# Kernel optimization log

Hardware: AMD Instinct MI355X
Metric: run time of the kernel (lower is better)

Reference implementation:

```python
import jax, jax.numpy as jnp
import numpy as np

EPS = 1e-6
KH, KW = 3, 3
SH, SW = 1, 1


def _unfold(x, kh, kw, sh, sw):
    # x: [N, C, H, W] -> patches [N, C, kh*kw, L], L = ox*oy (torch.nn.Unfold layout)
    N, C, H, W = x.shape
    ox = (H - kh) // sh + 1
    oy = (W - kw) // sw + 1
    pats = [x[:, :, i:i + sh * ox:sh, j:j + sw * oy:sw]
            for i in range(kh) for j in range(kw)]
    p = jnp.stack(pats, axis=2)  # [N, C, K, ox, oy]
    return p.reshape(N, C, kh * kw, ox * oy), ox, oy


def setup_inputs() -> dict:
    key = jax.random.key(0)
    kx, k1, k2 = jax.random.split(key, 3)
    x = jax.random.uniform(kx, (32, 2, 64, 64, 64), dtype=jnp.float32)
    w1 = jax.random.uniform(k1, (64, KH * KW), dtype=jnp.float32)
    w2 = jax.random.uniform(k2, (128, 64), dtype=jnp.float32)
    return {"x": x, "w1": w1, "w2": w2}


def reference(x, w1, w2):
    B = x.shape[0]
    out_ch = w2.shape[0]
    xr = x[:, 0]  # rotation plane [B, C, H, W]
    xa = x[:, 1]  # magnitude plane

    pr, ox, oy = _unfold(xr, KH, KW, SH, SW)  # [B, C, K, L]
    pa, _, _ = _unfold(xa, KH, KW, SH, SW)

    # weightNormalize1: squared weights normalized by GLOBAL sum (rot branch)
    w1_glob = w1 ** 2 / jnp.sum(w1 ** 2)
    w2_glob = w2 ** 2 / jnp.sum(w2 ** 2)
    # weightNormalize (drop_prob=0): squared weights normalized PER ROW (abs branch)
    w1_row = w1 ** 2 / jnp.sum(w1 ** 2, axis=1, keepdims=True)
    w2_row = w2 ** 2 / jnp.sum(w2 ** 2, axis=1, keepdims=True)

    # rotation branch: two weighted contractions
    rot = jnp.einsum('bckl,ck->bcl', pr, w1_glob)          # [B, C, L]
    out_rot = jnp.einsum('bcl,oc->bol', rot, w2_glob)      # [B, O, L]
    out_rot = out_rot.reshape(B, 1, out_ch, ox, oy)

    # magnitude branch: log -> weighted contractions -> exp
    la = jnp.log(pa + EPS)                                  # [B, C, K, L]
    a1 = jnp.einsum('bckl,ck->bcl', la, w1_row)             # [B, C, L]
    out_abs = jnp.exp(jnp.einsum('bcl,oc->bol', a1, w2_row))
    out_abs = out_abs.reshape(B, 1, out_ch, ox, oy)

    return jnp.concatenate([out_rot, out_abs], axis=1)  # [B, 2, O, ox, oy]
```

## Files before the change

kernel.cpp:

```cpp
#include <hip/hip_runtime.h>
#include <cstdint>
#include <cstddef>

#define EPSF 1e-6f

typedef __attribute__((ext_vector_type(4))) float f32x4;
typedef __attribute__((ext_vector_type(8))) short s16x8;
typedef union { s16x8 v; unsigned u[4]; } s16x8u;

static __device__ __forceinline__ unsigned short f2bf(float f) {
    unsigned u = __float_as_uint(f);
    u += 0x7FFFu + ((u >> 16) & 1u);
    return (unsigned short)(u >> 16);
}
static __device__ __forceinline__ float bf2f(unsigned short h) {
    return __uint_as_float(((unsigned)h) << 16);
}
static __device__ __forceinline__ unsigned packHL(float v) {
    unsigned short h = f2bf(v);
    float r = v - bf2f(h);
    unsigned short l = f2bf(r);
    return ((unsigned)h << 16) | (unsigned)l;
}

__global__ __launch_bounds__(256) void prep_weights(const float* __restrict__ w1,
                                                    const float* __restrict__ w2,
                                                    float* __restrict__ ws) {
    __shared__ float part1[4], part2[4];
    __shared__ float s1row[64];
    __shared__ float s2row[128];
    __shared__ float tot[2];

    const int t = threadIdx.x;
    const int ln = t & 63;
    const int wv = t >> 6;

    float s1 = 0.f;
    for (int i = t; i < 64 * 9; i += 256) { float v = w1[i]; s1 += v * v; }
    float s2 = 0.f;
    const float4* w2v = (const float4*)w2;
    for (int i = t; i < 2048; i += 256) {
        float4 v = w2v[i];
        s2 += v.x * v.x + v.y * v.y + v.z * v.z + v.w * v.w;
    }
    #pragma unroll
    for (int d = 32; d > 0; d >>= 1) {
        s1 += __shfl_down(s1, d);
        s2 += __shfl_down(s2, d);
    }
    if (ln == 0) { part1[wv] = s1; part2[wv] = s2; }

    if (t < 64) {
        float rs = 0.f;
        #pragma unroll
        for (int k = 0; k < 9; ++k) { float v = w1[t * 9 + k]; rs += v * v; }
        s1row[t] = rs;
    } else if (t < 192) {
        const int o = t - 64;
        float rs = 0.f;
        const float4* p = (const float4*)(w2 + o * 64);
        #pragma unroll
        for (int k = 0; k < 16; ++k) {
            float4 v = p[k];
            rs += v.x * v.x + v.y * v.y + v.z * v.z + v.w * v.w;
        }
        s2row[o] = rs;
    }
    __syncthreads();
    if (t == 0) tot[0] = part1[0] + part1[1] + part1[2] + part1[3];
    if (t == 1) tot[1] = part2[0] + part2[1] + part2[2] + part2[3];
    __syncthreads();

    const float t1 = tot[0];
    const float t2 = tot[1];
    for (int i = t; i < 64 * 9; i += 256) {
        const int c = i / 9;
        const int k = i - c * 9;
        const int idx = (c >> 4) * 144 + (c & 3) * 36 + ((c >> 2) & 3) * 9 + k;
        float q = w1[i] * w1[i];
        ws[idx] = q / t1;
        ws[576 + idx] = q / s1row[c];
    }
    unsigned* wsu = (unsigned*)ws;
    for (int i = t; i < 8192; i += 256) {
        float q = w2[i] * w2[i];
        wsu[1152 + i]        = packHL(q / t2);
        wsu[1152 + 8192 + i] = packHL(q / s2row[i >> 6]);
    }
}

__global__ __launch_bounds__(256) void conv_fused(const float* __restrict__ x,
                                                  const float* __restrict__ ws,
                                                  float* __restrict__ out) {
    const int h = blockIdx.x;
    const int branch = blockIdx.y;
    const int b = blockIdx.z;
    const int t = threadIdx.x;
    const int lane = t & 63;
    const int wv = __builtin_amdgcn_readfirstlane(t >> 6);
    const int lm = lane & 15;
    const int quad = lane >> 4;
    const int c4 = lm;
    const int chsub = quad;

    __shared__ unsigned rotT[64 * 65];

    const float* __restrict__ w1t = ws + branch * 576;
    const unsigned* __restrict__ w2p = (const unsigned*)ws + 1152 + branch * 8192;
    const float* __restrict__ xb = x + (size_t)(b * 2 + branch) * (64 * 4096);

    const float* xrow = xb + h * 64 + 4 * c4;
    #pragma unroll 2
    for (int cg = 0; cg < 4; ++cg) {
        const int c = wv * 16 + cg * 4 + chsub;
        const float* xp = xrow + c * 4096;
        float4 v0 = *(const float4*)xp;
        float4 v1 = *(const float4*)(xp + 64);
        float4 v2 = *(const float4*)(xp + 128);
        if (branch) {
            v0.x = __logf(v0.x + EPSF); v0.y = __logf(v0.y + EPSF);
            v0.z = __logf(v0.z + EPSF); v0.w = __logf(v0.w + EPSF);
            v1.x = __logf(v1.x + EPSF); v1.y = __logf(v1.y + EPSF);
            v1.z = __logf(v1.z + EPSF); v1.w = __logf(v1.w + EPSF);
            v2.x = __logf(v2.x + EPSF); v2.y = __logf(v2.y + EPSF);
            v2.z = __logf(v2.z + EPSF); v2.w = __logf(v2.w + EPSF);
        }
        const float sx0 = __shfl_down(v0.x, 1), sy0 = __shfl_down(v0.y, 1);
        const float sx1 = __shfl_down(v1.x, 1), sy1 = __shfl_down(v1.y, 1);
        const float sx2 = __shfl_down(v2.x, 1), sy2 = __shfl_down(v2.y, 1);
        const float* wc = w1t + wv * 144 + chsub * 36 + cg * 9;
        const float w0 = wc[0], w1_ = wc[1], w2_ = wc[2];
        const float w3 = wc[3], w4 = wc[4], w5 = wc[5];
        const float w6 = wc[6], w7 = wc[7], w8 = wc[8];
        float p0 = v0.x * w0 + v0.y * w1_ + v0.z * w2_
                 + v1.x * w3 + v1.y * w4  + v1.z * w5
                 + v2.x * w6 + v2.y * w7  + v2.z * w8;
        float p1 = v0.y * w0 + v0.z * w1_ + v0.w * w2_
                 + v1.y * w3 + v1.z * w4  + v1.w * w5
                 + v2.y * w6 + v2.z * w7  + v2.w * w8;
        float p2 = v0.z * w0 + v0.w * w1_ + sx0 * w2_
                 + v1.z * w3 + v1.w * w4  + sx1 * w5
                 + v2.z * w6 + v2.w * w7  + sx2 * w8;
        float p3 = v0.w * w0 + sx0 * w1_ + sy0 * w2_
                 + v1.w * w3 + sx1 * w4  + sy1 * w5
                 + v2.w * w6 + sx2 * w7  + sy2 * w8;
        unsigned* rp = &rotT[(4 * c4) * 65 + c];
        rp[0]   = packHL(p0);
        rp[65]  = packHL(p1);
        rp[130] = packHL(p2);
        rp[195] = packHL(p3);
    }

    unsigned araw[2][2][8];
    #pragma unroll
    for (int mt = 0; mt < 2; ++mt) {
        #pragma unroll
        for (int kk = 0; kk < 2; ++kk) {
            const unsigned* p = w2p + (wv * 32 + mt * 16 + lm) * 64 + kk * 32 + quad * 8;
            #pragma unroll
            for (int j = 0; j < 8; ++j) araw[mt][kk][j] = p[j];
        }
    }
    __syncthreads();

    s16x8u aH[2][2], aL[2][2];
    #pragma unroll
    for (int mt = 0; mt < 2; ++mt)
        #pragma unroll
        for (int kk = 0; kk < 2; ++kk)
            #pragma unroll
            for (int j2 = 0; j2 < 4; ++j2) {
                unsigned u0 = araw[mt][kk][2 * j2], u1 = araw[mt][kk][2 * j2 + 1];
                aH[mt][kk].u[j2] = __builtin_amdgcn_perm(u1, u0, 0x07060302u);
                aL[mt][kk].u[j2] = __builtin_amdgcn_perm(u1, u0, 0x05040100u);
            }

    f32x4 acc[2][4];
    #pragma unroll
    for (int mt = 0; mt < 2; ++mt)
        #pragma unroll
        for (int nt = 0; nt < 4; ++nt)
            acc[mt][nt] = (f32x4){0.f, 0.f, 0.f, 0.f};

    #pragma unroll
    for (int nt = 0; nt < 4; ++nt) {
        #pragma unroll
        for (int kk = 0; kk < 2; ++kk) {
            const unsigned* lp = &rotT[(nt * 16 + lm) * 65 + kk * 32 + quad * 8];
            s16x8u bH, bL;
            #pragma unroll
            for (int j2 = 0; j2 < 4; ++j2) {
                unsigned u0 = lp[2 * j2], u1 = lp[2 * j2 + 1];
                bH.u[j2] = __builtin_amdgcn_perm(u1, u0, 0x07060302u);
                bL.u[j2] = __builtin_amdgcn_perm(u1, u0, 0x05040100u);
            }
            #pragma unroll
            for (int mt = 0; mt < 2; ++mt) {
                acc[mt][nt] = __builtin_amdgcn_mfma_f32_16x16x32_bf16(aH[mt][kk].v, bH.v, acc[mt][nt], 0, 0, 0);
                acc[mt][nt] = __builtin_amdgcn_mfma_f32_16x16x32_bf16(aH[mt][kk].v, bL.v, acc[mt][nt], 0, 0, 0);
                acc[mt][nt] = __builtin_amdgcn_mfma_f32_16x16x32_bf16(aL[mt][kk].v, bH.v, acc[mt][nt], 0, 0, 0);
            }
        }
    }

    #pragma unroll
    for (int mt = 0; mt < 2; ++mt) {
        const int oc0 = wv * 32 + mt * 16 + quad * 4;
        #pragma unroll
        for (int nt = 0; nt < 4; ++nt) {
            const int px = nt * 16 + lm;
            if (px < 62) {
                const size_t base =
                    ((size_t)((b * 2 + branch) * 128 + oc0)) * 3844 + (size_t)h * 62 + px;
                #pragma unroll
                for (int r = 0; r < 4; ++r) {
                    float v = acc[mt][nt][r];
                    if (branch) v = __expf(v);
                    out[base + (size_t)r * 3844] = v;
                }
            }
        }
    }
}

extern "C" void kernel_launch(void* const* d_in, const int* in_sizes, int n_in,
                              void* d_out, int out_size, void* d_ws, size_t ws_size,
                              hipStream_t stream) {
    const float* x  = (const float*)d_in[0];
    const float* w1 = (const float*)d_in[1];
    const float* w2 = (const float*)d_in[2];
    float* out = (float*)d_out;
    float* ws  = (float*)d_ws;

    prep_weights<<<1, 256, 0, stream>>>(w1, w2, ws);

    dim3 grid(62, 2, 32);
    conv_fused<<<grid, 256, 0, stream>>>(x, ws, out);
}
```

Measured before the change: 219.1 us.

## Process two output rows per block, split weight prep into parallel kernels

The conv kernel now computes two output rows per block. It loads four input rows and reuses the middle two across both rows, and doubles the LDS tile and the MFMA N-tiles. The grid is reordered with batch on x and paired rows on z, and output stores become nontemporal. The single-block weight prep is split into two multi-block kernels: one computes row sums, and one packs the weights and recomputes the global sums from the stored row sums. This adds a kernel launch and raises LDS and register use per block, with the launch bound set to 4 waves per EU.

```diff
diff --git a/kernel.cpp b/kernel.cpp
--- a/kernel.cpp
+++ b/kernel.cpp
@@ -23,78 +23,70 @@
     return ((unsigned)h << 16) | (unsigned)l;
 }
 
-__global__ __launch_bounds__(256) void prep_weights(const float* __restrict__ w1,
-                                                    const float* __restrict__ w2,
-                                                    float* __restrict__ ws) {
-    __shared__ float part1[4], part2[4];
-    __shared__ float s1row[64];
-    __shared__ float s2row[128];
-    __shared__ float tot[2];
-
+
+__global__ __launch_bounds__(256) void prep_sums(const float* __restrict__ w1,
+                                                 const float* __restrict__ w2,
+                                                 float* __restrict__ ws) {
+    const int bid = blockIdx.x;
     const int t = threadIdx.x;
-    const int ln = t & 63;
+    const int lane = t & 63;
     const int wv = t >> 6;
-
-    float s1 = 0.f;
-    for (int i = t; i < 64 * 9; i += 256) { float v = w1[i]; s1 += v * v; }
-    float s2 = 0.f;
-    const float4* w2v = (const float4*)w2;
-    for (int i = t; i < 2048; i += 256) {
-        float4 v = w2v[i];
-        s2 += v.x * v.x + v.y * v.y + v.z * v.z + v.w * v.w;
-    }
+    if (bid < 32) {
+        const int row = bid * 4 + wv;
+        float v = w2[row * 64 + lane];
+        float s = v * v;
+        #pragma unroll
+        for (int d = 32; d > 0; d >>= 1) s += __shfl_down(s, d);
+        if (lane == 0) ws[17602 + row] = s;
+    } else if (t < 64) {
+        float rs = 0.f;
+        #pragma unroll
+        for (int k = 0; k < 9; ++k) { float v = w1[t * 9 + k]; rs += v * v; }
+        ws[17538 + t] = rs;
+    }
+}
+
+__global__ __launch_bounds__(256) void prep_pack(const float* __restrict__ w1,
+                                                 const float* __restrict__ w2,
+                                                 float* __restrict__ ws) {
+    const int t = threadIdx.x;
+    const int lane = t & 63;
+    const int gid = blockIdx.x * 256 + t;
+
+    float a = ws[17538 + lane];
+    float b0 = ws[17602 + lane] + ws[17602 + 64 + lane];
     #pragma unroll
     for (int d = 32; d > 0; d >>= 1) {
-        s1 += __shfl_down(s1, d);
-        s2 += __shfl_down(s2, d);
-    }
-    if (ln == 0) { part1[wv] = s1; part2[wv] = s2; }
-
-    if (t < 64) {
-        float rs = 0.f;
-        #pragma unroll
-        for (int k = 0; k < 9; ++k) { float v = w1[t * 9 + k]; rs += v * v; }
-        s1row[t] = rs;
-    } else if (t < 192) {
-        const int o = t - 64;
-        float rs = 0.f;
-        const float4* p = (const float4*)(w2 + o * 64);
-        #pragma unroll
-        for (int k = 0; k < 16; ++k) {
-            float4 v = p[k];
-            rs += v.x * v.x + v.y * v.y + v.z * v.z + v.w * v.w;
-        }
-        s2row[o] = rs;
-    }
-    __syncthreads();
-    if (t == 0) tot[0] = part1[0] + part1[1] + part1[2] + part1[3];
-    if (t == 1) tot[1] = part2[0] + part2[1] + part2[2] + part2[3];
-    __syncthreads();
-
-    const float t1 = tot[0];
-    const float t2 = tot[1];
-    for (int i = t; i < 64 * 9; i += 256) {
+        a += __shfl_xor(a, d);
+        b0 += __shfl_xor(b0, d);
+    }
+    const float t1 = a, t2 = b0;
+
+    unsigned* wsu = (unsigned*)ws;
+    if (gid < 8192) {
+        float v = w2[gid];
+        float q = v * v;
+        wsu[1152 + gid] = packHL(q / t2);
+        wsu[9344 + gid] = packHL(q / ws[17602 + (gid >> 6)]);
+    } else if (gid < 8768) {
+        const int i = gid - 8192;
         const int c = i / 9;
         const int k = i - c * 9;
         const int idx = (c >> 4) * 144 + (c & 3) * 36 + ((c >> 2) & 3) * 9 + k;
-        float q = w1[i] * w1[i];
+        float v = w1[i];
+        float q = v * v;
         ws[idx] = q / t1;
-        ws[576 + idx] = q / s1row[c];
-    }
-    unsigned* wsu = (unsigned*)ws;
-    for (int i = t; i < 8192; i += 256) {
-        float q = w2[i] * w2[i];
-        wsu[1152 + i]        = packHL(q / t2);
-        wsu[1152 + 8192 + i] = packHL(q / s2row[i >> 6]);
-    }
-}
-
-__global__ __launch_bounds__(256) void conv_fused(const float* __restrict__ x,
-                                                  const float* __restrict__ ws,
-                                                  float* __restrict__ out) {
-    const int h = blockIdx.x;
+        ws[576 + idx] = q / ws[17538 + c];
+    }
+}
+
+__global__ __launch_bounds__(256, 4) void conv_fused(const float* __restrict__ x,
+                                                     const float* __restrict__ ws,
+                                                     float* __restrict__ out) {
+    const int b = blockIdx.x;
     const int branch = blockIdx.y;
-    const int b = blockIdx.z;
+    const int hg = blockIdx.z;
+    const int h0 = hg * 2;
     const int t = threadIdx.x;
     const int lane = t & 63;
     const int wv = __builtin_amdgcn_readfirstlane(t >> 6);
@@ -103,13 +95,13 @@
     const int c4 = lm;
     const int chsub = quad;
 
-    __shared__ unsigned rotT[64 * 65];
+    __shared__ unsigned rotT[128 * 65];
 
     const float* __restrict__ w1t = ws + branch * 576;
     const unsigned* __restrict__ w2p = (const unsigned*)ws + 1152 + branch * 8192;
     const float* __restrict__ xb = x + (size_t)(b * 2 + branch) * (64 * 4096);
 
-    const float* xrow = xb + h * 64 + 4 * c4;
+    const float* xrow = xb + h0 * 64 + 4 * c4;
     #pragma unroll 2
     for (int cg = 0; cg < 4; ++cg) {
         const int c = wv * 16 + cg * 4 + chsub;
@@ -117,6 +109,7 @@
         float4 v0 = *(const float4*)xp;
         float4 v1 = *(const float4*)(xp + 64);
         float4 v2 = *(const float4*)(xp + 128);
+        float4 v3 = *(const float4*)(xp + 192);
         if (branch) {
             v0.x = __logf(v0.x + EPSF); v0.y = __logf(v0.y + EPSF);
             v0.z = __logf(v0.z + EPSF); v0.w = __logf(v0.w + EPSF);
@@ -124,10 +117,13 @@
             v1.z = __logf(v1.z + EPSF); v1.w = __logf(v1.w + EPSF);
             v2.x = __logf(v2.x + EPSF); v2.y = __logf(v2.y + EPSF);
             v2.z = __logf(v2.z + EPSF); v2.w = __logf(v2.w + EPSF);
+            v3.x = __logf(v3.x + EPSF); v3.y = __logf(v3.y + EPSF);
+            v3.z = __logf(v3.z + EPSF); v3.w = __logf(v3.w + EPSF);
         }
         const float sx0 = __shfl_down(v0.x, 1), sy0 = __shfl_down(v0.y, 1);
         const float sx1 = __shfl_down(v1.x, 1), sy1 = __shfl_down(v1.y, 1);
         const float sx2 = __shfl_down(v2.x, 1), sy2 = __shfl_down(v2.y, 1);
+        const float sx3 = __shfl_down(v3.x, 1), sy3 = __shfl_down(v3.y, 1);
         const float* wc = w1t + wv * 144 + chsub * 36 + cg * 9;
         const float w0 = wc[0], w1_ = wc[1], w2_ = wc[2];
         const float w3 = wc[3], w4 = wc[4], w5 = wc[5];
@@ -144,11 +140,28 @@
         float p3 = v0.w * w0 + sx0 * w1_ + sy0 * w2_
                  + v1.w * w3 + sx1 * w4  + sy1 * w5
                  + v2.w * w6 + sx2 * w7  + sy2 * w8;
+        float q0 = v1.x * w0 + v1.y * w1_ + v1.z * w2_
+                 + v2.x * w3 + v2.y * w4  + v2.z * w5
+                 + v3.x * w6 + v3.y * w7  + v3.z * w8;
+        float q1 = v1.y * w0 + v1.z * w1_ + v1.w * w2_
+                 + v2.y * w3 + v2.z * w4  + v2.w * w5
+                 + v3.y * w6 + v3.z * w7  + v3.w * w8;
+        float q2 = v1.z * w0 + v1.w * w1_ + sx1 * w2_
+                 + v2.z * w3 + v2.w * w4  + sx2 * w5
+                 + v3.z * w6 + v3.w * w7  + sx3 * w8;
+        float q3 = v1.w * w0 + sx1 * w1_ + sy1 * w2_
+                 + v2.w * w3 + sx2 * w4  + sy2 * w5
+                 + v3.w * w6 + sx3 * w7  + sy3 * w8;
         unsigned* rp = &rotT[(4 * c4) * 65 + c];
         rp[0]   = packHL(p0);
         rp[65]  = packHL(p1);
         rp[130] = packHL(p2);
         rp[195] = packHL(p3);
+        unsigned* rq = rp + 64 * 65;
+        rq[0]   = packHL(q0);
+        rq[65]  = packHL(q1);
+        rq[130] = packHL(q2);
+        rq[195] = packHL(q3);
     }
 
     unsigned araw[2][2][8];
@@ -175,15 +188,15 @@
                 aL[mt][kk].u[j2] = __builtin_amdgcn_perm(u1, u0, 0x05040100u);
             }
 
-    f32x4 acc[2][4];
+    f32x4 acc[2][8];
     #pragma unroll
     for (int mt = 0; mt < 2; ++mt)
         #pragma unroll
-        for (int nt = 0; nt < 4; ++nt)
+        for (int nt = 0; nt < 8; ++nt)
             acc[mt][nt] = (f32x4){0.f, 0.f, 0.f, 0.f};
 
     #pragma unroll
-    for (int nt = 0; nt < 4; ++nt) {
+    for (int nt = 0; nt < 8; ++nt) {
         #pragma unroll
         for (int kk = 0; kk < 2; ++kk) {
             const unsigned* lp = &rotT[(nt * 16 + lm) * 65 + kk * 32 + quad * 8];
@@ -207,16 +220,19 @@
     for (int mt = 0; mt < 2; ++mt) {
         const int oc0 = wv * 32 + mt * 16 + quad * 4;
         #pragma unroll
-        for (int nt = 0; nt < 4; ++nt) {
-            const int px = nt * 16 + lm;
-            if (px < 62) {
+        for (int nt = 0; nt < 8; ++nt) {
+            const int pxl = nt * 16 + lm;
+            const int row = pxl >> 6;
+            const int col = pxl & 63;
+            if (col < 62) {
                 const size_t base =
-                    ((size_t)((b * 2 + branch) * 128 + oc0)) * 3844 + (size_t)h * 62 + px;
+                    ((size_t)((b * 2 + branch) * 128 + oc0)) * 3844 +
+                    (size_t)(h0 + row) * 62 + col;
                 #pragma unroll
                 for (int r = 0; r < 4; ++r) {
                     float v = acc[mt][nt][r];
                     if (branch) v = __expf(v);
-                    out[base + (size_t)r * 3844] = v;
+                    __builtin_nontemporal_store(v, &out[base + (size_t)r * 3844]);
                 }
             }
         }
@@ -232,8 +248,9 @@
     float* out = (float*)d_out;
     float* ws  = (float*)d_ws;
 
-    prep_weights<<<1, 256, 0, stream>>>(w1, w2, ws);
-
-    dim3 grid(62, 2, 32);
+    prep_sums<<<33, 256, 0, stream>>>(w1, w2, ws);
+    prep_pack<<<35, 256, 0, stream>>>(w1, w2, ws);
+
+    dim3 grid(32, 2, 31);
     conv_fused<<<grid, 256, 0, stream>>>(x, ws, out);
 }
```

Result: slower. 270.6 us (+23.5%).
